# Kernel optimization log

Hardware: AMD Instinct MI355X
Metric: run time of the kernel (lower is better)

Reference implementation:

```python
import jax, jax.numpy as jnp
import numpy as np

H = 256
T = 2048
B = 64


def setup_inputs() -> dict:
    key = jax.random.key(0)
    ks = jax.random.split(key, 10)
    s = 1.0 / np.sqrt(H)
    return {
        "x": jax.random.normal(ks[0], (T, B, H), dtype=jnp.float32),
        # AttentionLayer params
        "W_b": jax.random.normal(ks[1], (H, H), dtype=jnp.float32) * s,
        "b_b": jnp.zeros((H,), dtype=jnp.float32),
        "v_b": jax.random.normal(ks[2], (1, H), dtype=jnp.float32) * s,
        "W_e": jax.random.normal(ks[3], (H, 2 * H), dtype=jnp.float32) * s,
        "b_e": jnp.zeros((H,), dtype=jnp.float32),
        # LSTMCell params (PyTorch layout: [4H, H], gate order i,f,g,o)
        "W_ih": jax.random.uniform(ks[4], (4 * H, H), dtype=jnp.float32, minval=-s, maxval=s),
        "W_hh": jax.random.uniform(ks[5], (4 * H, H), dtype=jnp.float32, minval=-s, maxval=s),
        "b_ih": jax.random.uniform(ks[6], (4 * H,), dtype=jnp.float32, minval=-s, maxval=s),
        "b_hh": jax.random.uniform(ks[7], (4 * H,), dtype=jnp.float32, minval=-s, maxval=s),
    }


def reference(x, W_b, b_b, v_b, W_e, b_e, W_ih, W_hh, b_ih, b_hh):
    # x: [T, B, H]. Effective recurrence per timestep (inner per-sample loop in
    # the original is dead code: its output writes are overwritten and its
    # states start from zeros each iteration).
    def step(carry, xi):
        h, c = carry  # [B, H] each
        hc = jnp.concatenate([h, c], axis=1)  # [B, 2H]
        a = hc @ W_e.T + b_e                  # [B, H]
        b = xi @ W_b.T + b_b                  # [B, H]
        j = jnp.tanh(a + b) @ v_b.T           # [B, 1]
        w = jax.nn.softmax(j, axis=0) * xi    # softmax over batch dim, [B, H]
        gates = w @ W_ih.T + b_ih + h @ W_hh.T + b_hh  # [B, 4H]
        i_g, f_g, g_g, o_g = jnp.split(gates, 4, axis=1)
        c_new = jax.nn.sigmoid(f_g) * c + jax.nn.sigmoid(i_g) * jnp.tanh(g_g)
        h_new = jax.nn.sigmoid(o_g) * jnp.tanh(c_new)
        return (h_new, c_new), h_new

    Bn, Hn = x.shape[1], x.shape[2]
    init = (jnp.zeros((Bn, Hn), x.dtype), jnp.zeros((Bn, Hn), x.dtype))
    _, output = jax.lax.scan(step, init, x)  # [T, B, H]
    return output
```

## Files before the change

kernel.cpp:

```cpp
#include <hip/hip_runtime.h>
#include <math.h>

constexpr int H   = 256;
constexpr int B   = 64;
constexpr int T   = 2048;
constexpr int G   = 64;
constexpr int NTH = 512;
constexpr int HB  = H * B;
constexpr int W   = 2;

struct SharedMain {
    float wU[256][16];
    float wV[256][16];
    float wA[768][4];
    float U[64][17];
    float V[64][17];
    float ap[64][5];
    alignas(16) float outst[64][4];
    float jp[8][64];
    float bg[16];
    float ba[4];
    float v4[4];
    float s[64];
};
union SharedAll {
    SharedMain m;
    float tile[64][65];
};

__device__ __forceinline__ float sigmoidf_(float v) {
    return 1.0f / (1.0f + expf(-v));
}

__device__ __forceinline__ void fence_rel() { __builtin_amdgcn_fence(__ATOMIC_RELEASE, "agent"); }
__device__ __forceinline__ void fence_acq() { __builtin_amdgcn_fence(__ATOMIC_ACQUIRE, "agent"); }

__device__ __forceinline__ void arrive(unsigned* c) {
    fence_rel();
    __hip_atomic_fetch_add(c, 1u, __ATOMIC_RELAXED, __HIP_MEMORY_SCOPE_AGENT);
}
__device__ __forceinline__ void wait_for(unsigned* c, unsigned target) {
    while (__hip_atomic_load(c, __ATOMIC_RELAXED, __HIP_MEMORY_SCOPE_AGENT) < target)
        __builtin_amdgcn_s_sleep(1);
    fence_acq();
}

__global__ void __launch_bounds__(NTH, 1)
scan_kernel(const float* __restrict__ x,
            const float* __restrict__ W_b,  const float* __restrict__ b_b,
            const float* __restrict__ v_b,  const float* __restrict__ W_e,
            const float* __restrict__ b_e,  const float* __restrict__ W_ih,
            const float* __restrict__ W_hh, const float* __restrict__ b_ih,
            const float* __restrict__ b_hh,
            float* __restrict__ out, float* __restrict__ wsf)
{
    __shared__ SharedAll sh;
    const int tid = threadIdx.x;
    const int g   = blockIdx.x;

    unsigned* cnt = (unsigned*)wsf;
    unsigned* bar = cnt + 0;
    unsigned* dj0 = cnt + 16;
    unsigned* dj1 = cnt + 32;
    unsigned* dh0 = cnt + 48;
    unsigned* dh1 = cnt + 64;

    float* pJ = wsf + 128;
    float* hT = pJ + W * G * 64;
    float* cT = hT + HB;
    float* xT = out;

    for (int tl = g; tl < T * 4; tl += G) {
        const int t  = tl >> 2;
        const int kc = (tl & 3) << 6;
        __syncthreads();
        for (int q = tid; q < 1024; q += NTH) {
            const int r  = q >> 4;
            const int c4 = (q & 15) << 2;
            const float4 v = *(const float4*)(x + (size_t)t * HB + (size_t)r * H + kc + c4);
            sh.tile[r][c4 + 0] = v.x; sh.tile[r][c4 + 1] = v.y;
            sh.tile[r][c4 + 2] = v.z; sh.tile[r][c4 + 3] = v.w;
        }
        __syncthreads();
        for (int q = tid; q < 1024; q += NTH) {
            const int k  = q >> 4;
            const int b4 = (q & 15) << 2;
            float4 v;
            v.x = sh.tile[b4 + 0][k]; v.y = sh.tile[b4 + 1][k];
            v.z = sh.tile[b4 + 2][k]; v.w = sh.tile[b4 + 3][k];
            *(float4*)(xT + (size_t)t * HB + (size_t)(kc + k) * B + b4) = v;
        }
    }
    __syncthreads();

    for (int e = tid; e < 256 * 16; e += NTH) {
        const int k  = e >> 4;
        const int cl = e & 15;
        const int gate = cl >> 2, oi = cl & 3;
        const int row = gate * H + 4 * g + oi;
        sh.m.wU[k][cl] = W_ih[(size_t)row * H + k];
        sh.m.wV[k][cl] = W_hh[(size_t)row * H + k];
    }
    for (int e = tid; e < 768 * 4; e += NTH) {
        const int r = e >> 2;
        const int i = e & 3;
        const int col = 4 * g + i;
        float w;
        if (r < 512) w = W_e[(size_t)col * 512 + r];
        else         w = W_b[(size_t)col * 256 + (r - 512)];
        sh.m.wA[r][i] = w;
    }
    if (tid < 16) {
        const int gate = tid >> 2, oi = tid & 3;
        const int col = gate * H + 4 * g + oi;
        sh.m.bg[tid] = b_ih[col] + b_hh[col];
    }
    if (tid < 4) {
        sh.m.ba[tid] = b_e[4 * g + tid] + b_b[4 * g + tid];
        sh.m.v4[tid] = v_b[4 * g + tid];
    }
    hT[g * NTH + tid] = 0.0f;

    __threadfence_block();
    __syncthreads();
    if (tid == 0) { arrive(bar); wait_for(bar, (unsigned)G); }
    __syncthreads();

    const int wv = tid >> 6;
    const int b  = tid & 63;

    for (int t = 0; t < T; ++t) {
        const int slot = t & 1;
        unsigned* dj = slot ? dj1 : dj0;
        const unsigned tgt = (unsigned)G * ((unsigned)(t >> 1) + 1u);

        for (int e = tid; e < 64 * 17; e += NTH) { (&sh.m.U[0][0])[e] = 0.0f; (&sh.m.V[0][0])[e] = 0.0f; }
        for (int e = tid; e < 64 * 5; e += NTH) (&sh.m.ap[0][0])[e] = 0.0f;
        __syncthreads();

        {
            const int kw = wv << 5;
            const float* src = xT + (size_t)t * HB + (size_t)kw * B;
            float aU[16], aA[4];
            #pragma unroll
            for (int c = 0; c < 16; ++c) aU[c] = 0.0f;
            aA[0] = aA[1] = aA[2] = aA[3] = 0.0f;
            #pragma unroll 4
            for (int kk = 0; kk < 32; ++kk) {
                const float xv = src[kk * B + b];
                const float* wr = sh.m.wU[kw + kk];
                #pragma unroll
                for (int c = 0; c < 16; ++c) aU[c] = fmaf(xv, wr[c], aU[c]);
                const float* wa = sh.m.wA[512 + kw + kk];
                #pragma unroll
                for (int i = 0; i < 4; ++i) aA[i] = fmaf(xv, wa[i], aA[i]);
            }
            #pragma unroll
            for (int c = 0; c < 16; ++c) atomicAdd(&sh.m.U[b][c], aU[c]);
            #pragma unroll
            for (int i = 0; i < 4; ++i) atomicAdd(&sh.m.ap[b][i], aA[i]);
        }

        if (tid == 0 && t > 0) {
            unsigned* dh = ((t - 1) & 1) ? dh1 : dh0;
            wait_for(dh, (unsigned)G * ((unsigned)((t - 1) >> 1) + 1u));
        }
        __syncthreads();

        {
            const int kw = wv << 5;
            const float* sH = hT + (size_t)kw * B;
            const float* sC = cT + (size_t)kw * B;
            float aV[16], aA[4];
            #pragma unroll
            for (int c = 0; c < 16; ++c) aV[c] = 0.0f;
            aA[0] = aA[1] = aA[2] = aA[3] = 0.0f;
            #pragma unroll 4
            for (int kk = 0; kk < 32; ++kk) {
                const float hv = sH[kk * B + b];
                const float cv = sC[kk * B + b];
                const float* wr = sh.m.wV[kw + kk];
                #pragma unroll
                for (int c = 0; c < 16; ++c) aV[c] = fmaf(hv, wr[c], aV[c]);
                const float* waH = sh.m.wA[kw + kk];
                const float* waC = sh.m.wA[256 + kw + kk];
                #pragma unroll
                for (int i = 0; i < 4; ++i) aA[i] = fmaf(hv, waH[i], fmaf(cv, waC[i], aA[i]));
            }
            #pragma unroll
            for (int c = 0; c < 16; ++c) atomicAdd(&sh.m.V[b][c], aV[c]);
            #pragma unroll
            for (int i = 0; i < 4; ++i) atomicAdd(&sh.m.ap[b][i], aA[i]);
        }
        __syncthreads();

        if (tid < 64) {
            float pj = 0.0f;
            #pragma unroll
            for (int i = 0; i < 4; ++i)
                pj += tanhf(sh.m.ap[tid][i] + sh.m.ba[i]) * sh.m.v4[i];
            pJ[(size_t)slot * G * 64 + g * 64 + tid] = pj;
            __threadfence_block();
        }
        __syncthreads();
        if (tid == 0) { arrive(dj); wait_for(dj, tgt); }
        __syncthreads();

        {
            float jpart = 0.0f;
            const int base = wv * 8;
            const float* pjs = pJ + (size_t)slot * G * 64;
            #pragma unroll
            for (int gg = 0; gg < 8; ++gg) jpart += pjs[(base + gg) * 64 + b];
            sh.m.jp[wv][b] = jpart;
        }
        __syncthreads();
        if (tid < 64) {
            float jv = 0.0f;
            #pragma unroll
            for (int w = 0; w < 8; ++w) jv += sh.m.jp[w][tid];
            float mx = jv;
            #pragma unroll
            for (int off = 32; off; off >>= 1) mx = fmaxf(mx, __shfl_xor(mx, off));
            const float e = expf(jv - mx);
            float ssum = e;
            #pragma unroll
            for (int off = 32; off; off >>= 1) ssum += __shfl_xor(ssum, off);
            sh.m.s[tid] = e / ssum;
        }
        __syncthreads();

        if (tid < 256) {
            const int oi = tid >> 6;
            const int bb = tid & 63;
            const float sb = sh.m.s[bb];
            const float pI = fmaf(sb, sh.m.U[bb][0  + oi], sh.m.V[bb][0  + oi]) + sh.m.bg[0  + oi];
            const float pF = fmaf(sb, sh.m.U[bb][4  + oi], sh.m.V[bb][4  + oi]) + sh.m.bg[4  + oi];
            const float pG = fmaf(sb, sh.m.U[bb][8  + oi], sh.m.V[bb][8  + oi]) + sh.m.bg[8  + oi];
            const float pO = fmaf(sb, sh.m.U[bb][12 + oi], sh.m.V[bb][12 + oi]) + sh.m.bg[12 + oi];
            const int col = 4 * g + oi;
            const float cold = cT[col * B + bb];
            const float cnew = sigmoidf_(pF) * cold + sigmoidf_(pI) * tanhf(pG);
            const float hnew = sigmoidf_(pO) * tanhf(cnew);
            cT[col * B + bb] = cnew;
            hT[col * B + bb] = hnew;
            sh.m.outst[bb][oi] = hnew;
            __threadfence_block();
        }
        __syncthreads();
        if (tid == 0) arrive(slot ? dh1 : dh0);

        if (tid < 64) {
            const float4 v = *(const float4*)sh.m.outst[tid];
            *(float4*)(out + (size_t)t * HB + (size_t)tid * H + 4 * g) = v;
        }
    }
}

extern "C" void kernel_launch(void* const* d_in, const int* in_sizes, int n_in,
                              void* d_out, int out_size, void* d_ws, size_t ws_size,
                              hipStream_t stream) {
    const float* x    = (const float*)d_in[0];
    const float* W_b  = (const float*)d_in[1];
    const float* b_b  = (const float*)d_in[2];
    const float* v_b  = (const float*)d_in[3];
    const float* W_e  = (const float*)d_in[4];
    const float* b_e  = (const float*)d_in[5];
    const float* W_ih = (const float*)d_in[6];
    const float* W_hh = (const float*)d_in[7];
    const float* b_ih = (const float*)d_in[8];
    const float* b_hh = (const float*)d_in[9];
    float*    out = (float*)d_out;
    float*    wsf = (float*)d_ws;

    hipMemsetAsync(d_ws, 0, 512, stream);

    void* args[] = { &x, &W_b, &b_b, &v_b, &W_e, &b_e, &W_ih, &W_hh, &b_ih, &b_hh,
                     &out, &wsf };
    hipLaunchCooperativeKernel((void*)scan_kernel, dim3(G), dim3(NTH), args, 0, stream);
}
```

Before: 102.5 ms.

## Replace fenced grid barriers with per-step relaxed-atomic flags and local cell state

Each timestep now uses its own zero-initialised dj and dh counters, so waits check a fixed target of G. Release and acquire fences are replaced by relaxed agent-scope atomic loads and stores plus s_waitcnt vmcnt(0). The cell state c now stays in LDS, the per-wave partial reduction of pJ is folded into a single 64-term read loop, and h and c are prefetched into registers before the matvec. This cuts block-level barriers and fence costs on the serial critical path. The risk is relying on relaxed atomics for cross-CU visibility without fences, and the workspace footprint grows.

```diff
diff --git a/kernel.cpp b/kernel.cpp
--- a/kernel.cpp
+++ b/kernel.cpp
@@ -7,7 +7,13 @@
 constexpr int G   = 64;
 constexpr int NTH = 512;
 constexpr int HB  = H * B;
-constexpr int W   = 2;
+
+constexpr int OFF_BAR = 0;
+constexpr int OFF_DJ  = 16;
+constexpr int OFF_DH  = OFF_DJ + T * 8;
+constexpr int OFF_PJ  = OFF_DH + T * 8;
+constexpr int OFF_HT  = OFF_PJ + 2 * G * 64;
+constexpr int OFF_CT  = OFF_HT + HB;
 
 struct SharedMain {
     float wU[256][16];
@@ -17,7 +23,7 @@
     float V[64][17];
     float ap[64][5];
     alignas(16) float outst[64][4];
-    float jp[8][64];
+    float c_own[4][64];
     float bg[16];
     float ba[4];
     float v4[4];
@@ -32,18 +38,24 @@
     return 1.0f / (1.0f + expf(-v));
 }
 
+__device__ __forceinline__ unsigned ld_rlx_u32(const unsigned* p) {
+    return __hip_atomic_load(p, __ATOMIC_RELAXED, __HIP_MEMORY_SCOPE_AGENT);
+}
+__device__ __forceinline__ float ld_rlx_f32(const float* p) {
+    return __hip_atomic_load(p, __ATOMIC_RELAXED, __HIP_MEMORY_SCOPE_AGENT);
+}
+__device__ __forceinline__ void st_rlx_f32(float* p, float v) {
+    __hip_atomic_store(p, v, __ATOMIC_RELAXED, __HIP_MEMORY_SCOPE_AGENT);
+}
+__device__ __forceinline__ void add_rlx_u32(unsigned* p, unsigned v) {
+    __hip_atomic_fetch_add(p, v, __ATOMIC_RELAXED, __HIP_MEMORY_SCOPE_AGENT);
+}
+__device__ __forceinline__ void waitcnt_vm() {
+    asm volatile("s_waitcnt vmcnt(0)" ::: "memory");
+}
+
 __device__ __forceinline__ void fence_rel() { __builtin_amdgcn_fence(__ATOMIC_RELEASE, "agent"); }
 __device__ __forceinline__ void fence_acq() { __builtin_amdgcn_fence(__ATOMIC_ACQUIRE, "agent"); }
-
-__device__ __forceinline__ void arrive(unsigned* c) {
-    fence_rel();
-    __hip_atomic_fetch_add(c, 1u, __ATOMIC_RELAXED, __HIP_MEMORY_SCOPE_AGENT);
-}
-__device__ __forceinline__ void wait_for(unsigned* c, unsigned target) {
-    while (__hip_atomic_load(c, __ATOMIC_RELAXED, __HIP_MEMORY_SCOPE_AGENT) < target)
-        __builtin_amdgcn_s_sleep(1);
-    fence_acq();
-}
 
 __global__ void __launch_bounds__(NTH, 1)
 scan_kernel(const float* __restrict__ x,
@@ -59,15 +71,9 @@
     const int g   = blockIdx.x;
 
     unsigned* cnt = (unsigned*)wsf;
-    unsigned* bar = cnt + 0;
-    unsigned* dj0 = cnt + 16;
-    unsigned* dj1 = cnt + 32;
-    unsigned* dh0 = cnt + 48;
-    unsigned* dh1 = cnt + 64;
-
-    float* pJ = wsf + 128;
-    float* hT = pJ + W * G * 64;
-    float* cT = hT + HB;
+    float* pJ = wsf + OFF_PJ;
+    float* hT = wsf + OFF_HT;
+    float* cT = wsf + OFF_CT;
     float* xT = out;
 
     for (int tl = g; tl < T * 4; tl += G) {
@@ -119,20 +125,26 @@
         sh.m.ba[tid] = b_e[4 * g + tid] + b_b[4 * g + tid];
         sh.m.v4[tid] = v_b[4 * g + tid];
     }
+    if (tid < 256) sh.m.c_own[tid >> 6][tid & 63] = 0.0f;
     hT[g * NTH + tid] = 0.0f;
-
-    __threadfence_block();
+    cnt[OFF_DJ + g * NTH + tid] = 0u;
+
     __syncthreads();
-    if (tid == 0) { arrive(bar); wait_for(bar, (unsigned)G); }
+    if (tid == 0) {
+        fence_rel();
+        add_rlx_u32(cnt + OFF_BAR, 1u);
+        while (ld_rlx_u32(cnt + OFF_BAR) < (unsigned)G) __builtin_amdgcn_s_sleep(1);
+        fence_acq();
+    }
     __syncthreads();
 
     const int wv = tid >> 6;
     const int b  = tid & 63;
 
     for (int t = 0; t < T; ++t) {
-        const int slot = t & 1;
-        unsigned* dj = slot ? dj1 : dj0;
-        const unsigned tgt = (unsigned)G * ((unsigned)(t >> 1) + 1u);
+        unsigned* dj_t = cnt + OFF_DJ + t * 8;
+        unsigned* dh_t = cnt + OFF_DH + t * 8;
+        float*    pJs  = pJ + (size_t)(t & 1) * G * 64;
 
         for (int e = tid; e < 64 * 17; e += NTH) { (&sh.m.U[0][0])[e] = 0.0f; (&sh.m.V[0][0])[e] = 0.0f; }
         for (int e = tid; e < 64 * 5; e += NTH) (&sh.m.ap[0][0])[e] = 0.0f;
@@ -162,23 +174,29 @@
         }
 
         if (tid == 0 && t > 0) {
-            unsigned* dh = ((t - 1) & 1) ? dh1 : dh0;
-            wait_for(dh, (unsigned)G * ((unsigned)((t - 1) >> 1) + 1u));
+            unsigned* dh_p = cnt + OFF_DH + (t - 1) * 8;
+            while (ld_rlx_u32(dh_p) < (unsigned)G) __builtin_amdgcn_s_sleep(1);
         }
         __syncthreads();
 
         {
             const int kw = wv << 5;
-            const float* sH = hT + (size_t)kw * B;
-            const float* sC = cT + (size_t)kw * B;
+            const float* sH = hT + (size_t)kw * B + b;
+            const float* sC = cT + (size_t)kw * B + b;
+            float hreg[32], creg[32];
+            #pragma unroll
+            for (int kk = 0; kk < 32; ++kk) {
+                hreg[kk] = ld_rlx_f32(sH + kk * B);
+                creg[kk] = ld_rlx_f32(sC + kk * B);
+            }
             float aV[16], aA[4];
             #pragma unroll
             for (int c = 0; c < 16; ++c) aV[c] = 0.0f;
             aA[0] = aA[1] = aA[2] = aA[3] = 0.0f;
             #pragma unroll 4
             for (int kk = 0; kk < 32; ++kk) {
-                const float hv = sH[kk * B + b];
-                const float cv = sC[kk * B + b];
+                const float hv = hreg[kk];
+                const float cv = creg[kk];
                 const float* wr = sh.m.wV[kw + kk];
                 #pragma unroll
                 for (int c = 0; c < 16; ++c) aV[c] = fmaf(hv, wr[c], aV[c]);
@@ -199,26 +217,18 @@
             #pragma unroll
             for (int i = 0; i < 4; ++i)
                 pj += tanhf(sh.m.ap[tid][i] + sh.m.ba[i]) * sh.m.v4[i];
-            pJ[(size_t)slot * G * 64 + g * 64 + tid] = pj;
-            __threadfence_block();
-        }
-        __syncthreads();
-        if (tid == 0) { arrive(dj); wait_for(dj, tgt); }
-        __syncthreads();
-
-        {
-            float jpart = 0.0f;
-            const int base = wv * 8;
-            const float* pjs = pJ + (size_t)slot * G * 64;
-            #pragma unroll
-            for (int gg = 0; gg < 8; ++gg) jpart += pjs[(base + gg) * 64 + b];
-            sh.m.jp[wv][b] = jpart;
+            st_rlx_f32(pJs + g * 64 + tid, pj);
+            waitcnt_vm();
+            if (tid == 0) {
+                add_rlx_u32(dj_t, 1u);
+                while (ld_rlx_u32(dj_t) < (unsigned)G) __builtin_amdgcn_s_sleep(1);
+            }
         }
         __syncthreads();
         if (tid < 64) {
             float jv = 0.0f;
             #pragma unroll
-            for (int w = 0; w < 8; ++w) jv += sh.m.jp[w][tid];
+            for (int gg = 0; gg < 64; ++gg) jv += ld_rlx_f32(pJs + gg * 64 + tid);
             float mx = jv;
             #pragma unroll
             for (int off = 32; off; off >>= 1) mx = fmaxf(mx, __shfl_xor(mx, off));
@@ -238,19 +248,22 @@
             const float pF = fmaf(sb, sh.m.U[bb][4  + oi], sh.m.V[bb][4  + oi]) + sh.m.bg[4  + oi];
             const float pG = fmaf(sb, sh.m.U[bb][8  + oi], sh.m.V[bb][8  + oi]) + sh.m.bg[8  + oi];
             const float pO = fmaf(sb, sh.m.U[bb][12 + oi], sh.m.V[bb][12 + oi]) + sh.m.bg[12 + oi];
-            const int col = 4 * g + oi;
-            const float cold = cT[col * B + bb];
+            const float cold = sh.m.c_own[oi][bb];
             const float cnew = sigmoidf_(pF) * cold + sigmoidf_(pI) * tanhf(pG);
             const float hnew = sigmoidf_(pO) * tanhf(cnew);
-            cT[col * B + bb] = cnew;
-            hT[col * B + bb] = hnew;
+            sh.m.c_own[oi][bb] = cnew;
             sh.m.outst[bb][oi] = hnew;
-            __threadfence_block();
-        }
-        __syncthreads();
-        if (tid == 0) arrive(slot ? dh1 : dh0);
+        }
+        __syncthreads();
 
         if (tid < 64) {
+            #pragma unroll
+            for (int oi = 0; oi < 4; ++oi) {
+                st_rlx_f32(hT + (size_t)(4 * g + oi) * B + tid, sh.m.outst[tid][oi]);
+                st_rlx_f32(cT + (size_t)(4 * g + oi) * B + tid, sh.m.c_own[oi][tid]);
+            }
+            waitcnt_vm();
+            if (tid == 0) add_rlx_u32(dh_t, 1u);
             const float4 v = *(const float4*)sh.m.outst[tid];
             *(float4*)(out + (size_t)t * HB + (size_t)tid * H + 4 * g) = v;
         }
@@ -270,10 +283,10 @@
     const float* W_hh = (const float*)d_in[7];
     const float* b_ih = (const float*)d_in[8];
     const float* b_hh = (const float*)d_in[9];
-    float*    out = (float*)d_out;
-    float*    wsf = (float*)d_ws;
-
-    hipMemsetAsync(d_ws, 0, 512, stream);
+    float* out = (float*)d_out;
+    float* wsf = (float*)d_ws;
+
+    hipMemsetAsync(d_ws, 0, 64, stream);
 
     void* args[] = { &x, &W_b, &b_b, &v_b, &W_e, &b_e, &W_ih, &W_hh, &b_ih, &b_hh,
                      &out, &wsf };
```

New measurement: 95.87 ms. -6.5%, faster.
